# Optimization experiments

Hardware: AMD Instinct MI355X
Metric: run time of the kernel (lower is better)

The kernel has to match this reference:

```python
import jax, jax.numpy as jnp
import numpy as np

N_NODES = 50000
N_HEDGES = 10000
NNZ = 640000
D_IN, D_HID, D_OUT = 128, 128, 128


def _glorot(key, fan_in, fan_out):
    s = jnp.sqrt(6.0 / (fan_in + fan_out)).astype(jnp.float32)
    return jax.random.uniform(key, (fan_in, fan_out), jnp.float32, -s, s)


def setup_inputs() -> dict:
    key = jax.random.key(0)
    k_x, k_r, k_c, k_w1, k_w2 = jax.random.split(key, 5)
    x = jax.random.normal(k_x, (N_NODES, D_IN), jnp.float32)
    row = jax.random.randint(k_r, (NNZ,), 0, N_NODES)  # node indices
    col = jax.random.randint(k_c, (NNZ,), 0, N_HEDGES)  # hyperedge indices
    edge_index = jnp.stack([row, col]).astype(jnp.int64)
    return {
        "x": x,
        "edge_index": edge_index,
        "W1": _glorot(k_w1, D_IN, D_HID),
        "b1": jnp.zeros((D_HID,), jnp.float32),
        "W2": _glorot(k_w2, D_HID, D_OUT),
        "b2": jnp.zeros((D_OUT,), jnp.float32),
    }


def _hconv(x, W, b, row, col):
    # PyG HypergraphConv (no attention): out = D^{-1} H B^{-1} H^T (X W) + b
    xw = x @ W  # [N, F_out]
    ones = jnp.ones(row.shape[0], xw.dtype)
    deg_n = jax.ops.segment_sum(ones, row, num_segments=N_NODES)    # node degree D
    deg_e = jax.ops.segment_sum(ones, col, num_segments=N_HEDGES)   # hyperedge degree B
    d_inv = jnp.where(deg_n > 0, 1.0 / deg_n, 0.0)
    b_inv = jnp.where(deg_e > 0, 1.0 / deg_e, 0.0)
    # node -> hyperedge aggregation: m_e = B^{-1} sum_{i in e} (XW)_i
    m = jax.ops.segment_sum(xw[row], col, num_segments=N_HEDGES) * b_inv[:, None]
    # hyperedge -> node aggregation: out_i = D^{-1} sum_{e ni i} m_e
    out = jax.ops.segment_sum(m[col], row, num_segments=N_NODES) * d_inv[:, None]
    return out + b


def reference(x, edge_index, W1, b1, W2, b2):
    row, col = edge_index[0], edge_index[1]
    h = jax.nn.relu(_hconv(x, W1, b1, row, col))  # dropout inactive in eval
    return _hconv(h, W2, b2, row, col)
```

## Files before the change

### kernel.cpp

```cpp
#include <hip/hip_runtime.h>
#include <hip/hip_bf16.h>

#define D 128
#define N_HEDGES 10000
#define PART_CHUNKS 128
#define CAP_N 64
#define CAP_E 192
#define CSTRIDE 16

__device__ __forceinline__ float bf2f(ushort u) {
    union { unsigned int i; float f; } v; v.i = ((unsigned int)u) << 16; return v.f;
}
__device__ __forceinline__ ushort f2bf(float f) {
    union { float f; unsigned int i; } v; v.f = f;
    unsigned int r = v.i + 0x7FFFu + ((v.i >> 16) & 1u);
    return (ushort)(r >> 16);
}

__global__ __launch_bounds__(256) void f32_to_bf16(const float* __restrict__ in,
                                                   ushort* __restrict__ out, int n4) {
    int i = blockIdx.x * 256 + threadIdx.x;
    if (i < n4) {
        float4 v = ((const float4*)in)[i];
        ushort4 o;
        o.x = f2bf(v.x); o.y = f2bf(v.y); o.z = f2bf(v.z); o.w = f2bf(v.w);
        ((ushort4*)out)[i] = o;
    }
}

__global__ __launch_bounds__(256) void build_part(const int* __restrict__ row,
                                                  const int* __restrict__ col,
                                                  int* __restrict__ cnt_n,
                                                  int* __restrict__ cnt_e,
                                                  ushort* __restrict__ pad_n,
                                                  ushort* __restrict__ pad_e,
                                                  int nnz, int N, int E) {
    int xcd = blockIdx.x & 7;
    int chunk = blockIdx.x >> 3;
    int csz = (nnz + PART_CHUNKS - 1) / PART_CHUNKS;
    int lo = chunk * csz;
    int hi = min(lo + csz, nnz);
    int nlo = (int)((long)N * xcd >> 3), nhi = (int)((long)N * (xcd + 1) >> 3);
    int elo = (int)((long)E * xcd >> 3), ehi = (int)((long)E * (xcd + 1) >> 3);
    for (int i = lo + threadIdx.x; i < hi; i += 256) {
        int r = row[i], c = col[i];
        if (r >= nlo && r < nhi) {
            int pn = atomicAdd(&cnt_n[(size_t)r * CSTRIDE], 1);
            if (pn < CAP_N) pad_n[(size_t)r * CAP_N + pn] = (ushort)c;
        }
        if (c >= elo && c < ehi) {
            int pe = atomicAdd(&cnt_e[(size_t)c * CSTRIDE], 1);
            if (pe < CAP_E) pad_e[(size_t)c * CAP_E + pe] = (ushort)r;
        }
    }
}

__global__ __launch_bounds__(256, 2) void gemm128_bf(const float* __restrict__ X,
                                                     const float* __restrict__ W,
                                                     ushort* __restrict__ Y, int M) {
    __shared__ float Wl[D * D];
    __shared__ float Xl[32 * D];
    int t = threadIdx.x;
    int block_row = blockIdx.x * 32;

    const float4* W4 = (const float4*)W;
    float4* Wl4 = (float4*)Wl;
#pragma unroll
    for (int i = 0; i < 16; ++i) Wl4[t + 256 * i] = W4[t + 256 * i];

    int rows = M - block_row; if (rows > 32) rows = 32;
#pragma unroll
    for (int i = 0; i < 4; ++i) {
        int idx = t + 256 * i;
        int r = idx >> 5, c4 = idx & 31;
        float4 v = make_float4(0.f, 0.f, 0.f, 0.f);
        if (r < rows) v = ((const float4*)(X + (size_t)(block_row + r) * D))[c4];
        ((float4*)Xl)[idx] = v;
    }
    __syncthreads();

    int cp = t & 63;
    int rg = t >> 6;
    float2 acc[8];
#pragma unroll
    for (int r = 0; r < 8; ++r) acc[r] = make_float2(0.f, 0.f);

    const float* xbase = Xl + (rg * 8) * D;
#pragma unroll 2
    for (int k4 = 0; k4 < 32; ++k4) {
        float2 wv0 = ((const float2*)(Wl + (k4 * 4 + 0) * D))[cp];
        float2 wv1 = ((const float2*)(Wl + (k4 * 4 + 1) * D))[cp];
        float2 wv2 = ((const float2*)(Wl + (k4 * 4 + 2) * D))[cp];
        float2 wv3 = ((const float2*)(Wl + (k4 * 4 + 3) * D))[cp];
#pragma unroll
        for (int r = 0; r < 8; ++r) {
            float4 xv = ((const float4*)(xbase + r * D))[k4];
            acc[r].x += xv.x * wv0.x; acc[r].y += xv.x * wv0.y;
            acc[r].x += xv.y * wv1.x; acc[r].y += xv.y * wv1.y;
            acc[r].x += xv.z * wv2.x; acc[r].y += xv.z * wv2.y;
            acc[r].x += xv.w * wv3.x; acc[r].y += xv.w * wv3.y;
        }
    }
#pragma unroll
    for (int r = 0; r < 8; ++r) {
        int row = block_row + rg * 8 + r;
        if (row < M) {
            ushort2 o; o.x = f2bf(acc[r].x); o.y = f2bf(acc[r].y);
            ((ushort2*)(Y + (size_t)row * D))[cp] = o;
        }
    }
}

__global__ __launch_bounds__(256) void edge_agg(const ushort* __restrict__ src,
                                                const ushort* __restrict__ pad,
                                                const int* __restrict__ cnt,
                                                float* __restrict__ dst, int nseg) {
    int w = (blockIdx.x * 256 + threadIdx.x) >> 6;
    int lane = threadIdx.x & 63;
    if (w >= nseg) return;
    int len = min(cnt[(size_t)w * CSTRIDE], CAP_E);
    const ushort* list = pad + (size_t)w * CAP_E;
    int half = lane >> 5;
    int c4 = lane & 31;
    float4 a0 = make_float4(0.f, 0.f, 0.f, 0.f);
    float4 a1 = make_float4(0.f, 0.f, 0.f, 0.f);
    int i = 0;
#pragma unroll 2
    for (; i + 4 <= len; i += 4) {
        int r0 = list[i + half];
        int r1 = list[i + 2 + half];
        ushort4 u0 = ((const ushort4*)(src + (size_t)r0 * D))[c4];
        ushort4 u1 = ((const ushort4*)(src + (size_t)r1 * D))[c4];
        a0.x += bf2f(u0.x); a0.y += bf2f(u0.y); a0.z += bf2f(u0.z); a0.w += bf2f(u0.w);
        a1.x += bf2f(u1.x); a1.y += bf2f(u1.y); a1.z += bf2f(u1.z); a1.w += bf2f(u1.w);
    }
    if (i + 2 <= len) {
        int r = list[i + half];
        ushort4 u = ((const ushort4*)(src + (size_t)r * D))[c4];
        a0.x += bf2f(u.x); a0.y += bf2f(u.y); a0.z += bf2f(u.z); a0.w += bf2f(u.w);
        i += 2;
    }
    if (i < len && half == 0) {
        int r = list[i];
        ushort4 u = ((const ushort4*)(src + (size_t)r * D))[c4];
        a1.x += bf2f(u.x); a1.y += bf2f(u.y); a1.z += bf2f(u.z); a1.w += bf2f(u.w);
    }
    a0.x += a1.x; a0.y += a1.y; a0.z += a1.z; a0.w += a1.w;
    a0.x += __shfl_xor(a0.x, 32);
    a0.y += __shfl_xor(a0.y, 32);
    a0.z += __shfl_xor(a0.z, 32);
    a0.w += __shfl_xor(a0.w, 32);
    if (half == 0) {
        float sc = (len > 0) ? (1.0f / (float)len) : 0.0f;
        ((float4*)(dst + (size_t)w * D))[c4] =
            make_float4(a0.x * sc, a0.y * sc, a0.z * sc, a0.w * sc);
    }
}

template <bool RELU>
__global__ __launch_bounds__(256) void node_agg(const ushort* __restrict__ src,
                                                const ushort* __restrict__ pad,
                                                const int* __restrict__ cnt,
                                                const float* __restrict__ bias,
                                                void* __restrict__ dst, int nseg) {
    int w = (blockIdx.x * 256 + threadIdx.x) >> 6;
    int lane = threadIdx.x & 63;
    if (w >= nseg) return;
    int len = min(cnt[(size_t)w * CSTRIDE], CAP_N);
    const ushort* list = pad + (size_t)w * CAP_N;
    int half = lane >> 5;
    int c4 = lane & 31;
    float4 a0 = make_float4(0.f, 0.f, 0.f, 0.f);
    float4 a1 = make_float4(0.f, 0.f, 0.f, 0.f);
    int i = 0;
#pragma unroll 2
    for (; i + 4 <= len; i += 4) {
        int r0 = list[i + half];
        int r1 = list[i + 2 + half];
        ushort4 u0 = ((const ushort4*)(src + (size_t)r0 * D))[c4];
        ushort4 u1 = ((const ushort4*)(src + (size_t)r1 * D))[c4];
        a0.x += bf2f(u0.x); a0.y += bf2f(u0.y); a0.z += bf2f(u0.z); a0.w += bf2f(u0.w);
        a1.x += bf2f(u1.x); a1.y += bf2f(u1.y); a1.z += bf2f(u1.z); a1.w += bf2f(u1.w);
    }
    if (i + 2 <= len) {
        int r = list[i + half];
        ushort4 u = ((const ushort4*)(src + (size_t)r * D))[c4];
        a0.x += bf2f(u.x); a0.y += bf2f(u.y); a0.z += bf2f(u.z); a0.w += bf2f(u.w);
        i += 2;
    }
    if (i < len && half == 0) {
        int r = list[i];
        ushort4 u = ((const ushort4*)(src + (size_t)r * D))[c4];
        a1.x += bf2f(u.x); a1.y += bf2f(u.y); a1.z += bf2f(u.z); a1.w += bf2f(u.w);
    }
    a0.x += a1.x; a0.y += a1.y; a0.z += a1.z; a0.w += a1.w;
    a0.x += __shfl_xor(a0.x, 32);
    a0.y += __shfl_xor(a0.y, 32);
    a0.z += __shfl_xor(a0.z, 32);
    a0.w += __shfl_xor(a0.w, 32);
    if (half == 0) {
        float sc = (len > 0) ? (1.0f / (float)len) : 0.0f;
        float4 bv = ((const float4*)bias)[c4];
        float ox = a0.x * sc + bv.x;
        float oy = a0.y * sc + bv.y;
        float oz = a0.z * sc + bv.z;
        float ow = a0.w * sc + bv.w;
        if (RELU) {
            ox = fmaxf(ox, 0.f); oy = fmaxf(oy, 0.f);
            oz = fmaxf(oz, 0.f); ow = fmaxf(ow, 0.f);
            ushort4 o;
            o.x = f2bf(ox); o.y = f2bf(oy); o.z = f2bf(oz); o.w = f2bf(ow);
            ((ushort4*)((ushort*)dst + (size_t)w * D))[c4] = o;
        } else {
            ((float4*)((float*)dst + (size_t)w * D))[c4] = make_float4(ox, oy, oz, ow);
        }
    }
}

extern "C" void kernel_launch(void* const* d_in, const int* in_sizes, int n_in,
                              void* d_out, int out_size, void* d_ws, size_t ws_size,
                              hipStream_t stream) {
    const float* x  = (const float*)d_in[0];
    const int*   ei = (const int*)d_in[1];
    const float* W1 = (const float*)d_in[2];
    const float* b1 = (const float*)d_in[3];
    const float* W2 = (const float*)d_in[4];
    const float* b2 = (const float*)d_in[5];
    float* out = (float*)d_out;

    const int NNZ = in_sizes[1] / 2;
    const int N   = in_sizes[0] / D;
    const int E   = N_HEDGES;

    const int* row = ei;
    const int* col = ei + NNZ;

    char* p = (char*)d_ws;
    auto alloc = [&](size_t bytes) {
        char* r = p;
        p += (bytes + 255) & ~(size_t)255;
        return r;
    };
    float*  s     = (float*)alloc(sizeof(float) * (size_t)E * D);
    ushort* m_bf  = (ushort*)alloc(sizeof(ushort) * (size_t)E * D);
    ushort* xh    = (ushort*)alloc(sizeof(ushort) * (size_t)N * D);
    ushort* pad_n = (ushort*)alloc(sizeof(ushort) * (size_t)N * CAP_N);
    ushort* pad_e = (ushort*)alloc(sizeof(ushort) * (size_t)E * CAP_E);
    char*   zstart = p;
    int*    cnt_n = (int*)alloc(sizeof(int) * (size_t)N * CSTRIDE);
    int*    cnt_e = (int*)alloc(sizeof(int) * (size_t)E * CSTRIDE);
    size_t  zbytes = (size_t)(p - zstart);
    ushort* hh = (ushort*)d_out;

    hipMemsetAsync(zstart, 0, zbytes, stream);

    build_part<<<8 * PART_CHUNKS, 256, 0, stream>>>(row, col, cnt_n, cnt_e,
                                                    pad_n, pad_e, NNZ, N, E);
    f32_to_bf16<<<(N * D / 4 + 255) / 256, 256, 0, stream>>>(x, xh, N * D / 4);

    int gemm_blocks = (E + 31) / 32;
    int eblk = (E + 3) / 4;
    int nblk = (N + 3) / 4;

    edge_agg<<<eblk, 256, 0, stream>>>(xh, pad_e, cnt_e, s, E);
    gemm128_bf<<<gemm_blocks, 256, 0, stream>>>(s, W1, m_bf, E);
    node_agg<true><<<nblk, 256, 0, stream>>>(m_bf, pad_n, cnt_n, b1, hh, N);

    edge_agg<<<eblk, 256, 0, stream>>>(hh, pad_e, cnt_e, s, E);
    gemm128_bf<<<gemm_blocks, 256, 0, stream>>>(s, W2, m_bf, E);
    node_agg<false><<<nblk, 256, 0, stream>>>(m_bf, pad_n, cnt_n, b2, out, N);
}
```

Measured before the change: 262.3 us.

## Widen gather loads to 16 bytes and fuse bf16 conversion into partition build

Gather-aggregation kernels now have each lane load a uint4 (8 bf16 values), so a 64-lane wave covers four neighbor rows per step instead of two. Partial sums are combined with two xor shuffles. The separate f32-to-bf16 conversion kernel is folded into the build_part kernel as a grid-stride loop, and the partition chunk count is doubled. The aim is fewer, wider memory transactions and one fewer kernel launch, at the cost of more accumulator registers and an extra shuffle stage.

```diff
diff --git a/kernel.cpp b/kernel.cpp
--- a/kernel.cpp
+++ b/kernel.cpp
@@ -3,29 +3,21 @@
 
 #define D 128
 #define N_HEDGES 10000
-#define PART_CHUNKS 128
+#define PART_CHUNKS 256
 #define CAP_N 64
 #define CAP_E 192
 #define CSTRIDE 16
 
-__device__ __forceinline__ float bf2f(ushort u) {
-    union { unsigned int i; float f; } v; v.i = ((unsigned int)u) << 16; return v.f;
+__device__ __forceinline__ float bf_lo(unsigned int u) {
+    union { unsigned int i; float f; } v; v.i = u << 16; return v.f;
+}
+__device__ __forceinline__ float bf_hi(unsigned int u) {
+    union { unsigned int i; float f; } v; v.i = u & 0xFFFF0000u; return v.f;
 }
 __device__ __forceinline__ ushort f2bf(float f) {
     union { float f; unsigned int i; } v; v.f = f;
     unsigned int r = v.i + 0x7FFFu + ((v.i >> 16) & 1u);
     return (ushort)(r >> 16);
-}
-
-__global__ __launch_bounds__(256) void f32_to_bf16(const float* __restrict__ in,
-                                                   ushort* __restrict__ out, int n4) {
-    int i = blockIdx.x * 256 + threadIdx.x;
-    if (i < n4) {
-        float4 v = ((const float4*)in)[i];
-        ushort4 o;
-        o.x = f2bf(v.x); o.y = f2bf(v.y); o.z = f2bf(v.z); o.w = f2bf(v.w);
-        ((ushort4*)out)[i] = o;
-    }
 }
 
 __global__ __launch_bounds__(256) void build_part(const int* __restrict__ row,
@@ -34,6 +26,8 @@
                                                   int* __restrict__ cnt_e,
                                                   ushort* __restrict__ pad_n,
                                                   ushort* __restrict__ pad_e,
+                                                  const float* __restrict__ x,
+                                                  ushort* __restrict__ xh,
                                                   int nnz, int N, int E) {
     int xcd = blockIdx.x & 7;
     int chunk = blockIdx.x >> 3;
@@ -53,6 +47,14 @@
             if (pe < CAP_E) pad_e[(size_t)c * CAP_E + pe] = (ushort)r;
         }
     }
+    int n4 = N * (D / 4);
+    int nthreads = 8 * PART_CHUNKS * 256;
+    for (int i = blockIdx.x * 256 + threadIdx.x; i < n4; i += nthreads) {
+        float4 v = ((const float4*)x)[i];
+        ushort4 o;
+        o.x = f2bf(v.x); o.y = f2bf(v.y); o.z = f2bf(v.z); o.w = f2bf(v.w);
+        ((ushort4*)xh)[i] = o;
+    }
 }
 
 __global__ __launch_bounds__(256, 2) void gemm128_bf(const float* __restrict__ X,
@@ -109,6 +111,13 @@
             ((ushort2*)(Y + (size_t)row * D))[cp] = o;
         }
     }
+}
+
+__device__ __forceinline__ void acc_row(float* a, uint4 u) {
+    a[0] += bf_lo(u.x); a[1] += bf_hi(u.x);
+    a[2] += bf_lo(u.y); a[3] += bf_hi(u.y);
+    a[4] += bf_lo(u.z); a[5] += bf_hi(u.z);
+    a[6] += bf_lo(u.w); a[7] += bf_hi(u.w);
 }
 
 __global__ __launch_bounds__(256) void edge_agg(const ushort* __restrict__ src,
@@ -120,40 +129,33 @@
     if (w >= nseg) return;
     int len = min(cnt[(size_t)w * CSTRIDE], CAP_E);
     const ushort* list = pad + (size_t)w * CAP_E;
-    int half = lane >> 5;
-    int c4 = lane & 31;
-    float4 a0 = make_float4(0.f, 0.f, 0.f, 0.f);
-    float4 a1 = make_float4(0.f, 0.f, 0.f, 0.f);
+    int q = lane >> 4;
+    int c8 = lane & 15;
+    float a[8];
+#pragma unroll
+    for (int j = 0; j < 8; ++j) a[j] = 0.f;
     int i = 0;
 #pragma unroll 2
     for (; i + 4 <= len; i += 4) {
-        int r0 = list[i + half];
-        int r1 = list[i + 2 + half];
-        ushort4 u0 = ((const ushort4*)(src + (size_t)r0 * D))[c4];
-        ushort4 u1 = ((const ushort4*)(src + (size_t)r1 * D))[c4];
-        a0.x += bf2f(u0.x); a0.y += bf2f(u0.y); a0.z += bf2f(u0.z); a0.w += bf2f(u0.w);
-        a1.x += bf2f(u1.x); a1.y += bf2f(u1.y); a1.z += bf2f(u1.z); a1.w += bf2f(u1.w);
-    }
-    if (i + 2 <= len) {
-        int r = list[i + half];
-        ushort4 u = ((const ushort4*)(src + (size_t)r * D))[c4];
-        a0.x += bf2f(u.x); a0.y += bf2f(u.y); a0.z += bf2f(u.z); a0.w += bf2f(u.w);
-        i += 2;
-    }
-    if (i < len && half == 0) {
-        int r = list[i];
-        ushort4 u = ((const ushort4*)(src + (size_t)r * D))[c4];
-        a1.x += bf2f(u.x); a1.y += bf2f(u.y); a1.z += bf2f(u.z); a1.w += bf2f(u.w);
-    }
-    a0.x += a1.x; a0.y += a1.y; a0.z += a1.z; a0.w += a1.w;
-    a0.x += __shfl_xor(a0.x, 32);
-    a0.y += __shfl_xor(a0.y, 32);
-    a0.z += __shfl_xor(a0.z, 32);
-    a0.w += __shfl_xor(a0.w, 32);
-    if (half == 0) {
+        int r = list[i + q];
+        uint4 u = ((const uint4*)(src + (size_t)r * D))[c8];
+        acc_row(a, u);
+    }
+    if (q < len - i) {
+        int r = list[i + q];
+        uint4 u = ((const uint4*)(src + (size_t)r * D))[c8];
+        acc_row(a, u);
+    }
+#pragma unroll
+    for (int j = 0; j < 8; ++j) {
+        a[j] += __shfl_xor(a[j], 16);
+        a[j] += __shfl_xor(a[j], 32);
+    }
+    if (q == 0) {
         float sc = (len > 0) ? (1.0f / (float)len) : 0.0f;
-        ((float4*)(dst + (size_t)w * D))[c4] =
-            make_float4(a0.x * sc, a0.y * sc, a0.z * sc, a0.w * sc);
+        float4* o = (float4*)(dst + (size_t)w * D + c8 * 8);
+        o[0] = make_float4(a[0] * sc, a[1] * sc, a[2] * sc, a[3] * sc);
+        o[1] = make_float4(a[4] * sc, a[5] * sc, a[6] * sc, a[7] * sc);
     }
 }
 
@@ -168,51 +170,50 @@
     if (w >= nseg) return;
     int len = min(cnt[(size_t)w * CSTRIDE], CAP_N);
     const ushort* list = pad + (size_t)w * CAP_N;
-    int half = lane >> 5;
-    int c4 = lane & 31;
-    float4 a0 = make_float4(0.f, 0.f, 0.f, 0.f);
-    float4 a1 = make_float4(0.f, 0.f, 0.f, 0.f);
+    int q = lane >> 4;
+    int c8 = lane & 15;
+    float a[8];
+#pragma unroll
+    for (int j = 0; j < 8; ++j) a[j] = 0.f;
     int i = 0;
 #pragma unroll 2
     for (; i + 4 <= len; i += 4) {
-        int r0 = list[i + half];
-        int r1 = list[i + 2 + half];
-        ushort4 u0 = ((const ushort4*)(src + (size_t)r0 * D))[c4];
-        ushort4 u1 = ((const ushort4*)(src + (size_t)r1 * D))[c4];
-        a0.x += bf2f(u0.x); a0.y += bf2f(u0.y); a0.z += bf2f(u0.z); a0.w += bf2f(u0.w);
-        a1.x += bf2f(u1.x); a1.y += bf2f(u1.y); a1.z += bf2f(u1.z); a1.w += bf2f(u1.w);
-    }
-    if (i + 2 <= len) {
-        int r = list[i + half];
-        ushort4 u = ((const ushort4*)(src + (size_t)r * D))[c4];
-        a0.x += bf2f(u.x); a0.y += bf2f(u.y); a0.z += bf2f(u.z); a0.w += bf2f(u.w);
-        i += 2;
-    }
-    if (i < len && half == 0) {
-        int r = list[i];
-        ushort4 u = ((const ushort4*)(src + (size_t)r * D))[c4];
-        a1.x += bf2f(u.x); a1.y += bf2f(u.y); a1.z += bf2f(u.z); a1.w += bf2f(u.w);
-    }
-    a0.x += a1.x; a0.y += a1.y; a0.z += a1.z; a0.w += a1.w;
-    a0.x += __shfl_xor(a0.x, 32);
-    a0.y += __shfl_xor(a0.y, 32);
-    a0.z += __shfl_xor(a0.z, 32);
-    a0.w += __shfl_xor(a0.w, 32);
-    if (half == 0) {
+        int r = list[i + q];
+        uint4 u = ((const uint4*)(src + (size_t)r * D))[c8];
+        acc_row(a, u);
+    }
+    if (q < len - i) {
+        int r = list[i + q];
+        uint4 u = ((const uint4*)(src + (size_t)r * D))[c8];
+        acc_row(a, u);
+    }
+#pragma unroll
+    for (int j = 0; j < 8; ++j) {
+        a[j] += __shfl_xor(a[j], 16);
+        a[j] += __shfl_xor(a[j], 32);
+    }
+    if (q == 0) {
         float sc = (len > 0) ? (1.0f / (float)len) : 0.0f;
-        float4 bv = ((const float4*)bias)[c4];
-        float ox = a0.x * sc + bv.x;
-        float oy = a0.y * sc + bv.y;
-        float oz = a0.z * sc + bv.z;
-        float ow = a0.w * sc + bv.w;
+        const float4* bv = (const float4*)(bias + c8 * 8);
+        float4 b0 = bv[0], b1 = bv[1];
+        float o0 = a[0] * sc + b0.x, o1 = a[1] * sc + b0.y;
+        float o2 = a[2] * sc + b0.z, o3 = a[3] * sc + b0.w;
+        float o4 = a[4] * sc + b1.x, o5 = a[5] * sc + b1.y;
+        float o6 = a[6] * sc + b1.z, o7 = a[7] * sc + b1.w;
         if (RELU) {
-            ox = fmaxf(ox, 0.f); oy = fmaxf(oy, 0.f);
-            oz = fmaxf(oz, 0.f); ow = fmaxf(ow, 0.f);
-            ushort4 o;
-            o.x = f2bf(ox); o.y = f2bf(oy); o.z = f2bf(oz); o.w = f2bf(ow);
-            ((ushort4*)((ushort*)dst + (size_t)w * D))[c4] = o;
+            o0 = fmaxf(o0, 0.f); o1 = fmaxf(o1, 0.f);
+            o2 = fmaxf(o2, 0.f); o3 = fmaxf(o3, 0.f);
+            o4 = fmaxf(o4, 0.f); o5 = fmaxf(o5, 0.f);
+            o6 = fmaxf(o6, 0.f); o7 = fmaxf(o7, 0.f);
+            ushort4 u0, u1;
+            u0.x = f2bf(o0); u0.y = f2bf(o1); u0.z = f2bf(o2); u0.w = f2bf(o3);
+            u1.x = f2bf(o4); u1.y = f2bf(o5); u1.z = f2bf(o6); u1.w = f2bf(o7);
+            ushort4* o = (ushort4*)((ushort*)dst + (size_t)w * D + c8 * 8);
+            o[0] = u0; o[1] = u1;
         } else {
-            ((float4*)((float*)dst + (size_t)w * D))[c4] = make_float4(ox, oy, oz, ow);
+            float4* o = (float4*)((float*)dst + (size_t)w * D + c8 * 8);
+            o[0] = make_float4(o0, o1, o2, o3);
+            o[1] = make_float4(o4, o5, o6, o7);
         }
     }
 }
@@ -255,8 +256,7 @@
     hipMemsetAsync(zstart, 0, zbytes, stream);
 
     build_part<<<8 * PART_CHUNKS, 256, 0, stream>>>(row, col, cnt_n, cnt_e,
-                                                    pad_n, pad_e, NNZ, N, E);
-    f32_to_bf16<<<(N * D / 4 + 255) / 256, 256, 0, stream>>>(x, xh, N * D / 4);
+                                                    pad_n, pad_e, x, xh, NNZ, N, E);
 
     int gemm_blocks = (E + 31) / 32;
     int eblk = (E + 3) / 4;
```

After: 254.5 us. -2.9%, faster.
